# Optimization experiments

Hardware: AMD Instinct MI355X
Metric: run time of the kernel (lower is better)

## Reference

```python
import jax, jax.numpy as jnp
import numpy as np

MIN_V, MAX_V = 1e-7, 10.0
POWER = 2.0
N_NODES = 200000


def _hyper_layer(H, edges, W, b):
    """One HyperTensorGraphConvolution layer (full-neighborhood branch).

    H: [N, d] node signals; edges: [E, S] node indices per hyperedge.
    For each (edge, node_i): power-mean over the other S-1 nodes of the edge,
    divided by (S-1), accumulated onto node_i; then row-normalize and linear.
    """
    N, d = H.shape
    E, S = edges.shape
    H = jnp.clip(H, MIN_V, MAX_V)
    P = H ** POWER                                   # [N, d]
    g = P[edges]                                     # [E, S, d] gather
    edge_sum = g.sum(axis=1, keepdims=True)          # [E, 1, d]
    neigh_mean = (edge_sum - g) / (S - 1)            # exclude self, /(len(nodes)-1)
    contrib = neigh_mean ** (1.0 / POWER)            # [E, S, d]
    add = jax.ops.segment_sum(contrib.reshape(E * S, d),
                              edges.reshape(-1), num_segments=N)
    new_signal = H + add
    # row-normalize (rowsum > 0 because H >= 1e-7)
    rowsum = new_signal.sum(axis=1)
    r_inv = jnp.where(jnp.isfinite(1.0 / rowsum), 1.0 / rowsum, 0.0)
    AH = new_signal * r_inv[:, None]
    return AH @ W + b


def setup_inputs() -> dict:
    key = jax.random.key(0)
    k1, k2, k3, k4, k5, k6 = jax.random.split(key, 6)
    d, h, c = 128, 16, 40
    H = jax.random.uniform(k1, (N_NODES, d), dtype=jnp.float32)
    edges = jax.random.randint(k2, (40000, 16), 0, N_NODES, dtype=jnp.int64)
    std1 = 1.0 / np.sqrt(h)
    std2 = 1.0 / np.sqrt(c)
    W1 = jax.random.uniform(k3, (d, h), jnp.float32, -std1, std1)
    b1 = jax.random.uniform(k4, (h,), jnp.float32, -std1, std1)
    W2 = jax.random.uniform(k5, (h, c), jnp.float32, -std2, std2)
    b2 = jax.random.uniform(k6, (c,), jnp.float32, -std2, std2)
    return {"H": H, "W1": W1, "b1": b1, "W2": W2, "b2": b2, "edges": edges}


def reference(H, W1, b1, W2, b2, edges):
    # layer 1 + relu (dropout is identity in eval mode)
    x = jax.nn.relu(_hyper_layer(H, edges, W1, b1))
    # layer 2
    return _hyper_layer(x, edges, W2, b2)
```

## Files before the change

### kernel.cpp

```cpp
#include <hip/hip_runtime.h>

#define MIN_V 1e-7f
#define MAX_V 10.0f
#define INV15 (1.0f/15.0f)
#define CAP 32

typedef _Float16 half2v __attribute__((ext_vector_type(2)));
typedef _Float16 half4v __attribute__((ext_vector_type(4)));
typedef _Float16 half8v __attribute__((ext_vector_type(8)));

static __device__ __forceinline__ float clipv(float v){
    return fminf(fmaxf(v, MIN_V), MAX_V);
}
static __device__ __forceinline__ half2v shflx1(half2v v){
    int i = __builtin_bit_cast(int, v);
    i = __shfl_xor(i, 1, 64);
    return __builtin_bit_cast(half2v, i);
}

__global__ __launch_bounds__(256) void ch_stream(const float* __restrict__ H,
                                                 _Float16* __restrict__ CH, int total8){
    int stride = gridDim.x*256;
    for (int i = blockIdx.x*256 + threadIdx.x; i < total8; i += stride){
        const float4* p = (const float4*)(H + (size_t)i*8);
        float4 a = p[0], b = p[1];
        half8v o;
        o[0]=(_Float16)clipv(a.x); o[1]=(_Float16)clipv(a.y);
        o[2]=(_Float16)clipv(a.z); o[3]=(_Float16)clipv(a.w);
        o[4]=(_Float16)clipv(b.x); o[5]=(_Float16)clipv(b.y);
        o[6]=(_Float16)clipv(b.z); o[7]=(_Float16)clipv(b.w);
        *(half8v*)(CH + (size_t)i*8) = o;
    }
}

__global__ void build_lists(const int* __restrict__ edges, int* __restrict__ cnt,
                            unsigned short* __restrict__ lists, int total){
    int i = blockIdx.x*256 + threadIdx.x;
    if (i >= total) return;
    int node = edges[i];
    int p = atomicAdd(&cnt[node], 1);
    if (p < CAP) lists[(size_t)node*CAP + p] = (unsigned short)(i >> 4);
}

__global__ __launch_bounds__(256) void es_l1(const _Float16* __restrict__ CH,
                                             const int* __restrict__ edges,
                                             _Float16* __restrict__ ES1s, int E){
    int tid = threadIdx.x;
    int sub = tid & 15;
    int e = blockIdx.x*16 + (tid >> 4);
    if (e >= E) return;
    int nid = edges[(size_t)e*16 + sub];
    float s[8];
    #pragma unroll
    for (int j=0;j<8;++j) s[j] = 0.f;
    #pragma unroll
    for (int t=0;t<16;++t){
        int idx = __shfl(nid, t, 16);
        half8v v = *(const half8v*)(CH + (size_t)idx*128 + sub*8);
        #pragma unroll
        for (int j=0;j<8;++j){ float f = (float)v[j]; s[j] += f*f; }
    }
    half8v o;
    #pragma unroll
    for (int j=0;j<8;++j) o[j] = (_Float16)(s[j]*INV15);
    *(half8v*)(ES1s + (size_t)e*128 + sub*8) = o;
}

__global__ __launch_bounds__(256) void fused_l1(
    const _Float16* __restrict__ CH, const _Float16* __restrict__ ES1s,
    const int* __restrict__ cnt, const unsigned short* __restrict__ lists,
    const float* __restrict__ W1, const float* __restrict__ b1,
    _Float16* __restrict__ X, int N, int EZERO){
    __shared__ _Float16 snw[8*128];
    int tid = threadIdx.x;
    int wave = tid >> 6, lane = tid & 63;

    int q = lane >> 4, h = lane & 15;
    half2v w2[16];
    #pragma unroll
    for (int i=0;i<16;++i){
        w2[i][0] = (_Float16)W1[(q*32+2*i  )*16 + h];
        w2[i][1] = (_Float16)W1[(q*32+2*i+1)*16 + h];
    }
    const half2v ones = {(_Float16)1.f, (_Float16)1.f};
    float bv = b1[h];

    int hw = tid >> 5;
    int k32 = tid & 31;
    int dq = k32 * 4;
    int nb = blockIdx.x * 8;

    const _Float16 i15 = (_Float16)INV15;
    const half4v i15v = {i15, i15, i15, i15};
    const half4v z4 = {(_Float16)0.f,(_Float16)0.f,(_Float16)0.f,(_Float16)0.f};

    int n = nb + hw;
    if (n < N){
        int len = cnt[n]; if (len > CAP) len = CAP;
        int myid = (int)lists[(size_t)n*CAP + k32];
        myid = (k32 < len) ? myid : EZERO;

        half4v hv = *(const half4v*)(CH + (size_t)n*128 + dq);
        half4v p16 = (hv * hv) * i15v;

        half4v acc = z4;
        for (int k0=0;k0<len;k0+=4){
            int e0 = __shfl(myid, k0,   32);
            int e1 = __shfl(myid, k0+1, 32);
            int e2 = __shfl(myid, k0+2, 32);
            int e3 = __shfl(myid, k0+3, 32);
            half4v v0 = *(const half4v*)(ES1s + (size_t)e0*128 + dq);
            half4v v1 = *(const half4v*)(ES1s + (size_t)e1*128 + dq);
            half4v v2 = *(const half4v*)(ES1s + (size_t)e2*128 + dq);
            half4v v3 = *(const half4v*)(ES1s + (size_t)e3*128 + dq);
            acc = acc + __builtin_elementwise_sqrt(__builtin_elementwise_max(v0 - p16, z4));
            acc = acc + __builtin_elementwise_sqrt(__builtin_elementwise_max(v1 - p16, z4));
            acc = acc + __builtin_elementwise_sqrt(__builtin_elementwise_max(v2 - p16, z4));
            acc = acc + __builtin_elementwise_sqrt(__builtin_elementwise_max(v3 - p16, z4));
        }
        *(half4v*)&snw[hw*128 + dq] = hv + acc;
    }
    __syncthreads();

    #pragma unroll
    for (int r=0;r<2;++r){
        int nl = wave*2 + r;
        int n2 = nb + nl;
        if (n2 >= N) continue;
        float acc = 0.f, rs = 0.f;
        #pragma unroll
        for (int j=0;j<8;++j){
            half4v v = *(const half4v*)&snw[nl*128 + q*32 + j*4];
            half2v lo = {v[0], v[1]}, hi = {v[2], v[3]};
            acc = __builtin_amdgcn_fdot2(lo, w2[j*2  ], acc, false);
            acc = __builtin_amdgcn_fdot2(hi, w2[j*2+1], acc, false);
            rs  = __builtin_amdgcn_fdot2(lo, ones, rs, false);
            rs  = __builtin_amdgcn_fdot2(hi, ones, rs, false);
        }
        acc += __shfl_xor(acc, 16, 64);
        rs  += __shfl_xor(rs , 16, 64);
        acc += __shfl_xor(acc, 32, 64);
        rs  += __shfl_xor(rs , 32, 64);
        if (q == 0){
            float o = acc * __builtin_amdgcn_rcpf(rs) + bv;
            X[(size_t)n2*16 + h] = (_Float16)fmaxf(o, 0.f);
        }
    }
}

__global__ __launch_bounds__(256) void es_l2(const _Float16* __restrict__ X,
                                             const int* __restrict__ edges,
                                             _Float16* __restrict__ ES2s, int E){
    int t = blockIdx.x*256 + threadIdx.x;
    int e = t >> 2, dq = (t & 3)*4;
    if (e >= E) return;
    const int* row = edges + (size_t)e*16;
    const _Float16 c7 = (_Float16)1e-7f;
    const half4v c7v = {c7, c7, c7, c7};
    float s0=0.f, s1=0.f, s2=0.f, s3=0.f;
    #pragma unroll
    for (int s=0;s<16;++s){
        half4v v = *(const half4v*)(X + (size_t)row[s]*16 + dq);
        v = __builtin_elementwise_max(v, c7v);
        float f0=(float)v[0], f1=(float)v[1], f2=(float)v[2], f3=(float)v[3];
        s0 += f0*f0; s1 += f1*f1; s2 += f2*f2; s3 += f3*f3;
    }
    half4v o;
    o[0]=(_Float16)(s0*INV15); o[1]=(_Float16)(s1*INV15);
    o[2]=(_Float16)(s2*INV15); o[3]=(_Float16)(s3*INV15);
    *(half4v*)(ES2s + (size_t)e*16 + dq) = o;
}

__global__ __launch_bounds__(256) void node_l2(
    const _Float16* __restrict__ X, const _Float16* __restrict__ ES2s,
    const int* __restrict__ cnt, const unsigned short* __restrict__ lists,
    const float* __restrict__ W2, const float* __restrict__ b2,
    float* __restrict__ out, int N, int EZERO){
    __shared__ half2v sW2h[8*40];
    __shared__ float sb[40];
    for (int i=threadIdx.x;i<320;i+=256){
        int d2 = i/40, c = i - d2*40;
        half2v wp;
        wp[0] = (_Float16)W2[(2*d2  )*40 + c];
        wp[1] = (_Float16)W2[(2*d2+1)*40 + c];
        sW2h[i] = wp;
    }
    if (threadIdx.x < 40) sb[threadIdx.x] = b2[threadIdx.x];
    __syncthreads();
    int t = blockIdx.x*256 + threadIdx.x;
    int n = t >> 1, p = t & 1;
    if (n >= N) return;

    const _Float16 c7 = (_Float16)1e-7f;
    const half8v c7v = {c7,c7,c7,c7,c7,c7,c7,c7};
    const half8v z8 = {(_Float16)0.f,(_Float16)0.f,(_Float16)0.f,(_Float16)0.f,
                       (_Float16)0.f,(_Float16)0.f,(_Float16)0.f,(_Float16)0.f};
    const _Float16 i15 = (_Float16)INV15;
    const half8v i15v = {i15,i15,i15,i15,i15,i15,i15,i15};

    half8v xh = *(const half8v*)(X + (size_t)n*16 + p*8);
    xh = __builtin_elementwise_max(xh, c7v);
    half8v ps = (xh*xh)*i15v;

    float xc[8], ad[8];
    #pragma unroll
    for (int d=0;d<8;++d){ xc[d]=(float)xh[d]; ad[d]=0.f; }

    int len = cnt[n]; if (len > CAP) len = CAP;
    const unsigned short* lrow = lists + (size_t)n*CAP;
    for (int k0=0;k0<len;k0+=4){
        int e0 = (int)lrow[k0];
        int e1 = (k0+1 < len) ? (int)lrow[k0+1] : EZERO;
        int e2 = (k0+2 < len) ? (int)lrow[k0+2] : EZERO;
        int e3 = (k0+3 < len) ? (int)lrow[k0+3] : EZERO;
        half8v r0 = *(const half8v*)(ES2s + (size_t)e0*16 + p*8);
        half8v r1 = *(const half8v*)(ES2s + (size_t)e1*16 + p*8);
        half8v r2 = *(const half8v*)(ES2s + (size_t)e2*16 + p*8);
        half8v r3 = *(const half8v*)(ES2s + (size_t)e3*16 + p*8);
        half8v s0 = __builtin_elementwise_sqrt(__builtin_elementwise_max(r0-ps, z8));
        half8v s1 = __builtin_elementwise_sqrt(__builtin_elementwise_max(r1-ps, z8));
        half8v s2 = __builtin_elementwise_sqrt(__builtin_elementwise_max(r2-ps, z8));
        half8v s3 = __builtin_elementwise_sqrt(__builtin_elementwise_max(r3-ps, z8));
        #pragma unroll
        for (int d=0;d<8;++d)
            ad[d] += ((float)s0[d] + (float)s1[d]) + ((float)s2[d] + (float)s3[d]);
    }
    float rsl = 0.f;
    float nw[8];
    #pragma unroll
    for (int d=0;d<8;++d){ nw[d] = xc[d] + ad[d]; rsl += nw[d]; }
    float rs = rsl + __shfl_xor(rsl, 1, 64);
    float rinv = __builtin_amdgcn_rcpf(rs);

    half2v mine[4], oth[4];
    #pragma unroll
    for (int i=0;i<4;++i){
        mine[i][0] = (_Float16)nw[2*i];
        mine[i][1] = (_Float16)nw[2*i+1];
        oth[i] = shflx1(mine[i]);
    }
    half2v all8[8];
    #pragma unroll
    for (int i=0;i<4;++i){
        all8[4*p + i]     = mine[i];
        all8[4*(1-p) + i] = oth[i];
    }

    float ob[20];
    #pragma unroll
    for (int c=0;c<20;++c){
        int col = p*20 + c;
        float acc = 0.f;
        #pragma unroll
        for (int d2=0;d2<8;++d2)
            acc = __builtin_amdgcn_fdot2(all8[d2], sW2h[d2*40+col], acc, false);
        ob[c] = rinv*acc + sb[col];
    }
    float4* op = (float4*)(out + (size_t)n*40 + p*20);
    #pragma unroll
    for (int j=0;j<5;++j) op[j] = ((float4*)ob)[j];
}

extern "C" void kernel_launch(void* const* d_in, const int* in_sizes, int n_in,
                              void* d_out, int out_size, void* d_ws, size_t ws_size,
                              hipStream_t stream){
    (void)n_in; (void)out_size; (void)ws_size;
    const float* H  = (const float*)d_in[0];
    const float* W1 = (const float*)d_in[1];
    const float* b1 = (const float*)d_in[2];
    const float* W2 = (const float*)d_in[3];
    const float* b2 = (const float*)d_in[4];
    const int* edges = (const int*)d_in[5];
    float* out = (float*)d_out;

    const int N = in_sizes[0] / 128;
    const int E = in_sizes[5] / 16;
    const int total = E * 16;
    const int total8 = N * 128 / 8;

    char* ws = (char*)d_ws;
    size_t off = 0;
    _Float16* CH   = (_Float16*)(ws + off);
    _Float16* ES2s = (_Float16*)(ws + off);
    off += (size_t)N*128*sizeof(_Float16);
    _Float16* ES1s = (_Float16*)(ws + off); off += (size_t)(E+1)*128*sizeof(_Float16);
    _Float16* X    = (_Float16*)(ws + off); off += (size_t)N*16*sizeof(_Float16);
    int* cnt = (int*)(ws + off); off += (size_t)N*sizeof(int);
    unsigned short* lists = (unsigned short*)(ws + off);
    off += (size_t)N*CAP*sizeof(unsigned short);

    hipMemsetAsync(cnt, 0, (size_t)N*sizeof(int), stream);
    hipMemsetAsync(ES1s + (size_t)E*128, 0, 128*sizeof(_Float16), stream);
    ch_stream<<<2048, 256, 0, stream>>>(H, CH, total8);
    build_lists<<<(total+255)/256, 256, 0, stream>>>(edges, cnt, lists, total);
    es_l1<<<(E+15)/16, 256, 0, stream>>>(CH, edges, ES1s, E);
    fused_l1<<<(N+7)/8, 256, 0, stream>>>(CH, ES1s, cnt, lists, W1, b1, X, N, E);
    hipMemsetAsync(ES2s + (size_t)E*16, 0, 16*sizeof(_Float16), stream);
    es_l2<<<(E*4+255)/256, 256, 0, stream>>>(X, edges, ES2s, E);
    node_l2<<<(N*2+255)/256, 256, 0, stream>>>(X, ES2s, cnt, lists, W2, b2, out, N, E);
}
```

Before: 197.3 us.

## Split layer-1 edge sums into four feature-quarter slices and process quarters sequentially

Edge-sum buffer ES1 is stored as four separate 32-channel slices, each holding all edges, instead of one 128-channel row per edge. fused_l1 now gives each node 8 threads that walk the four quarters one after another, and each block covers 32 nodes instead of 8. The goal is a smaller working set per gather pass so the random edge gathers hit L2 more often. The trade-off is fewer threads per node, less memory-level parallelism, more loop iterations and four times the shared memory per block.

New measurement: 207.9 us. +5.4%, slower.

```diff
diff --git a/kernel.cpp b/kernel.cpp
--- a/kernel.cpp
+++ b/kernel.cpp
@@ -8,6 +8,7 @@
 typedef _Float16 half2v __attribute__((ext_vector_type(2)));
 typedef _Float16 half4v __attribute__((ext_vector_type(4)));
 typedef _Float16 half8v __attribute__((ext_vector_type(8)));
+typedef unsigned short ushort4v __attribute__((ext_vector_type(4)));
 
 static __device__ __forceinline__ float clipv(float v){
     return fminf(fmaxf(v, MIN_V), MAX_V);
@@ -44,7 +45,7 @@
 
 __global__ __launch_bounds__(256) void es_l1(const _Float16* __restrict__ CH,
                                              const int* __restrict__ edges,
-                                             _Float16* __restrict__ ES1s, int E){
+                                             _Float16* __restrict__ ES1q, int E){
     int tid = threadIdx.x;
     int sub = tid & 15;
     int e = blockIdx.x*16 + (tid >> 4);
@@ -63,15 +64,15 @@
     half8v o;
     #pragma unroll
     for (int j=0;j<8;++j) o[j] = (_Float16)(s[j]*INV15);
-    *(half8v*)(ES1s + (size_t)e*128 + sub*8) = o;
+    *(half8v*)(ES1q + ((size_t)(sub>>2)*(E+1) + e)*32 + (sub&3)*8) = o;
 }
 
 __global__ __launch_bounds__(256) void fused_l1(
-    const _Float16* __restrict__ CH, const _Float16* __restrict__ ES1s,
+    const _Float16* __restrict__ CH, const _Float16* __restrict__ ES1q,
     const int* __restrict__ cnt, const unsigned short* __restrict__ lists,
     const float* __restrict__ W1, const float* __restrict__ b1,
     _Float16* __restrict__ X, int N, int EZERO){
-    __shared__ _Float16 snw[8*128];
+    __shared__ _Float16 snw[32*128];
     int tid = threadIdx.x;
     int wave = tid >> 6, lane = tid & 63;
 
@@ -85,55 +86,63 @@
     const half2v ones = {(_Float16)1.f, (_Float16)1.f};
     float bv = b1[h];
 
-    int hw = tid >> 5;
-    int k32 = tid & 31;
-    int dq = k32 * 4;
-    int nb = blockIdx.x * 8;
+    int nl = tid >> 3;
+    int j  = tid & 7;
+    int nb = blockIdx.x * 32;
+    int n  = nb + nl;
 
     const _Float16 i15 = (_Float16)INV15;
     const half4v i15v = {i15, i15, i15, i15};
     const half4v z4 = {(_Float16)0.f,(_Float16)0.f,(_Float16)0.f,(_Float16)0.f};
-
-    int n = nb + hw;
+    const size_t srow = (size_t)(EZERO + 1) * 32;
+
     if (n < N){
         int len = cnt[n]; if (len > CAP) len = CAP;
-        int myid = (int)lists[(size_t)n*CAP + k32];
-        myid = (k32 < len) ? myid : EZERO;
-
-        half4v hv = *(const half4v*)(CH + (size_t)n*128 + dq);
-        half4v p16 = (hv * hv) * i15v;
-
-        half4v acc = z4;
-        for (int k0=0;k0<len;k0+=4){
-            int e0 = __shfl(myid, k0,   32);
-            int e1 = __shfl(myid, k0+1, 32);
-            int e2 = __shfl(myid, k0+2, 32);
-            int e3 = __shfl(myid, k0+3, 32);
-            half4v v0 = *(const half4v*)(ES1s + (size_t)e0*128 + dq);
-            half4v v1 = *(const half4v*)(ES1s + (size_t)e1*128 + dq);
-            half4v v2 = *(const half4v*)(ES1s + (size_t)e2*128 + dq);
-            half4v v3 = *(const half4v*)(ES1s + (size_t)e3*128 + dq);
-            acc = acc + __builtin_elementwise_sqrt(__builtin_elementwise_max(v0 - p16, z4));
-            acc = acc + __builtin_elementwise_sqrt(__builtin_elementwise_max(v1 - p16, z4));
-            acc = acc + __builtin_elementwise_sqrt(__builtin_elementwise_max(v2 - p16, z4));
-            acc = acc + __builtin_elementwise_sqrt(__builtin_elementwise_max(v3 - p16, z4));
+        ushort4v lv = *(const ushort4v*)(lists + (size_t)n*CAP + j*4);
+        int m0 = (j*4+0 < len) ? (int)lv[0] : EZERO;
+        int m1 = (j*4+1 < len) ? (int)lv[1] : EZERO;
+        int m2 = (j*4+2 < len) ? (int)lv[2] : EZERO;
+        int m3 = (j*4+3 < len) ? (int)lv[3] : EZERO;
+        int iters = (len + 3) >> 2;
+
+        #pragma unroll
+        for (int dq=0; dq<4; ++dq){
+            half4v hv = *(const half4v*)(CH + (size_t)n*128 + dq*32 + j*4);
+            half4v p16 = (hv * hv) * i15v;
+            const _Float16* slice = ES1q + (size_t)dq*srow;
+
+            half4v acc = z4;
+            for (int g=0; g<iters; ++g){
+                int e0 = __shfl(m0, g, 8);
+                int e1 = __shfl(m1, g, 8);
+                int e2 = __shfl(m2, g, 8);
+                int e3 = __shfl(m3, g, 8);
+                half4v v0 = *(const half4v*)(slice + (size_t)e0*32 + j*4);
+                half4v v1 = *(const half4v*)(slice + (size_t)e1*32 + j*4);
+                half4v v2 = *(const half4v*)(slice + (size_t)e2*32 + j*4);
+                half4v v3 = *(const half4v*)(slice + (size_t)e3*32 + j*4);
+                acc = acc + __builtin_elementwise_sqrt(__builtin_elementwise_max(v0 - p16, z4));
+                acc = acc + __builtin_elementwise_sqrt(__builtin_elementwise_max(v1 - p16, z4));
+                acc = acc + __builtin_elementwise_sqrt(__builtin_elementwise_max(v2 - p16, z4));
+                acc = acc + __builtin_elementwise_sqrt(__builtin_elementwise_max(v3 - p16, z4));
+            }
+            *(half4v*)&snw[nl*128 + dq*32 + j*4] = hv + acc;
         }
-        *(half4v*)&snw[hw*128 + dq] = hv + acc;
     }
     __syncthreads();
 
     #pragma unroll
-    for (int r=0;r<2;++r){
-        int nl = wave*2 + r;
-        int n2 = nb + nl;
+    for (int r=0;r<8;++r){
+        int nl2 = wave*8 + r;
+        int n2 = nb + nl2;
         if (n2 >= N) continue;
         float acc = 0.f, rs = 0.f;
         #pragma unroll
-        for (int j=0;j<8;++j){
-            half4v v = *(const half4v*)&snw[nl*128 + q*32 + j*4];
+        for (int jj=0;jj<8;++jj){
+            half4v v = *(const half4v*)&snw[nl2*128 + q*32 + jj*4];
             half2v lo = {v[0], v[1]}, hi = {v[2], v[3]};
-            acc = __builtin_amdgcn_fdot2(lo, w2[j*2  ], acc, false);
-            acc = __builtin_amdgcn_fdot2(hi, w2[j*2+1], acc, false);
+            acc = __builtin_amdgcn_fdot2(lo, w2[jj*2  ], acc, false);
+            acc = __builtin_amdgcn_fdot2(hi, w2[jj*2+1], acc, false);
             rs  = __builtin_amdgcn_fdot2(lo, ones, rs, false);
             rs  = __builtin_amdgcn_fdot2(hi, ones, rs, false);
         }
@@ -283,18 +292,19 @@
     _Float16* CH   = (_Float16*)(ws + off);
     _Float16* ES2s = (_Float16*)(ws + off);
     off += (size_t)N*128*sizeof(_Float16);
-    _Float16* ES1s = (_Float16*)(ws + off); off += (size_t)(E+1)*128*sizeof(_Float16);
+    _Float16* ES1q = (_Float16*)(ws + off); off += (size_t)4*(E+1)*32*sizeof(_Float16);
     _Float16* X    = (_Float16*)(ws + off); off += (size_t)N*16*sizeof(_Float16);
     int* cnt = (int*)(ws + off); off += (size_t)N*sizeof(int);
     unsigned short* lists = (unsigned short*)(ws + off);
     off += (size_t)N*CAP*sizeof(unsigned short);
 
     hipMemsetAsync(cnt, 0, (size_t)N*sizeof(int), stream);
-    hipMemsetAsync(ES1s + (size_t)E*128, 0, 128*sizeof(_Float16), stream);
+    for (int dq=0; dq<4; ++dq)
+        hipMemsetAsync(ES1q + ((size_t)dq*(E+1) + E)*32, 0, 32*sizeof(_Float16), stream);
     ch_stream<<<2048, 256, 0, stream>>>(H, CH, total8);
     build_lists<<<(total+255)/256, 256, 0, stream>>>(edges, cnt, lists, total);
-    es_l1<<<(E+15)/16, 256, 0, stream>>>(CH, edges, ES1s, E);
-    fused_l1<<<(N+7)/8, 256, 0, stream>>>(CH, ES1s, cnt, lists, W1, b1, X, N, E);
+    es_l1<<<(E+15)/16, 256, 0, stream>>>(CH, edges, ES1q, E);
+    fused_l1<<<(N+31)/32, 256, 0, stream>>>(CH, ES1q, cnt, lists, W1, b1, X, N, E);
     hipMemsetAsync(ES2s + (size_t)E*16, 0, 16*sizeof(_Float16), stream);
     es_l2<<<(E*4+255)/256, 256, 0, stream>>>(X, edges, ES2s, E);
     node_l2<<<(N*2+255)/256, 256, 0, stream>>>(X, ES2s, cnt, lists, W2, b2, out, N, E);
```
